# Kernel optimization log

Measured on AMD Instinct MI355X. Metric: run time of the kernel, lower is better.

Reference implementation:

```python
import jax, jax.numpy as jnp
import numpy as np

B, S, D_IN, H, G, HD = 1, 2048, 2048, 32, 8, 128
GS = H // G  # group_size = 4
D_OUT = H * HD  # 4096
EPS = 1e-6


def _rmsnorm(x, scale):
    # qwen3-compatible: compute in fp32 over last dim
    xf = x.astype(jnp.float32)
    var = jnp.mean(xf * xf, axis=-1, keepdims=True)
    return (xf * jax.lax.rsqrt(var + EPS) * scale).astype(x.dtype)


def _apply_rope(x, cos, sin):
    # x: [b, h, s, d]; cos/sin: [s, d]
    d2 = x.shape[-1] // 2
    x1, x2 = x[..., :d2], x[..., d2:]
    rotated = jnp.concatenate([-x2, x1], axis=-1)
    return (x * cos[None, None] + rotated * sin[None, None]).astype(x.dtype)


def setup_inputs() -> dict:
    key = jax.random.key(0)
    ks = jax.random.split(key, 8)
    x = jax.random.normal(ks[0], (B, S, D_IN), jnp.float32)
    mask = jnp.triu(jnp.ones((S, S), bool), k=1)  # causal: True = masked
    # RoPE tables [S, HD]
    inv_freq = 1.0 / (10000.0 ** (jnp.arange(0, HD, 2, dtype=jnp.float32) / HD))
    ang = jnp.arange(S, dtype=jnp.float32)[:, None] * inv_freq[None, :]
    ang = jnp.concatenate([ang, ang], axis=-1)
    cos, sin = jnp.cos(ang), jnp.sin(ang)
    std = 0.02
    Wq = jax.random.normal(ks[1], (D_IN, D_OUT), jnp.float32) * std
    Wk = jax.random.normal(ks[2], (D_IN, G * HD), jnp.float32) * std
    Wv = jax.random.normal(ks[3], (D_IN, G * HD), jnp.float32) * std
    Wo = jax.random.normal(ks[4], (D_OUT, D_IN), jnp.float32) * std
    q_scale = jnp.ones((HD,), jnp.float32)
    k_scale = jnp.ones((HD,), jnp.float32)
    return {"x": x, "mask": mask, "cos": cos, "sin": sin,
            "Wq": Wq, "Wk": Wk, "Wv": Wv, "Wo": Wo,
            "q_scale": q_scale, "k_scale": k_scale}


def reference(x, mask, cos, sin, Wq, Wk, Wv, Wo, q_scale, k_scale):
    b, s, _ = x.shape
    q = (x @ Wq).reshape(b, s, H, HD).transpose(0, 2, 1, 3)   # [b,H,s,hd]
    k = (x @ Wk).reshape(b, s, G, HD).transpose(0, 2, 1, 3)   # [b,G,s,hd]
    v = (x @ Wv).reshape(b, s, G, HD).transpose(0, 2, 1, 3)   # [b,G,s,hd]
    q = _rmsnorm(q, q_scale)
    k = _rmsnorm(k, k_scale)
    q = _apply_rope(q, cos[:s], sin[:s])
    k = _apply_rope(k, cos[:s], sin[:s])
    next_k, next_v = k, v  # cache (num_kv_groups heads)
    # GQA via broadcasting instead of repeat_interleave (same math)
    qg = q.reshape(b, G, GS, s, HD)
    scores = jnp.einsum('bgrsd,bgtd->bgrst', qg, k)           # [b,G,gs,s,s]
    scores = jnp.where(mask[None, None, None], -jnp.inf, scores)
    attn = jax.nn.softmax(scores / np.sqrt(HD).astype(np.float32), axis=-1)
    ctx = jnp.einsum('bgrst,bgtd->bgrsd', attn, v)            # [b,G,gs,s,hd]
    ctx = ctx.reshape(b, H, s, HD).transpose(0, 2, 1, 3).reshape(b, s, D_OUT)
    out = ctx @ Wo
    return out, next_k, next_v
```

## Files before the change

### kernel.cpp

```cpp
#include <hip/hip_runtime.h>

typedef unsigned short ushort_t;
typedef short short8 __attribute__((ext_vector_type(8)));
typedef float floatx4 __attribute__((ext_vector_type(4)));

#define S_LEN 2048
#define DIN   2048
#define NH    32
#define NG    8
#define HDIM  128
#define DOUT  4096
#define DKV   1024
#define QLD   6144

__device__ __forceinline__ float b2f(ushort_t u) {
  union { float f; unsigned u; } t; t.u = ((unsigned)u) << 16; return t.f;
}
__device__ __forceinline__ ushort_t f2b(float f) {
  union { float f; unsigned u; } t; t.f = f;
  unsigned v = t.u;
  v += 0x7FFFu + ((v >> 16) & 1u);
  return (ushort_t)(v >> 16);
}

__device__ __forceinline__ void glds16(const ushort_t* g, ushort_t* l) {
  __builtin_amdgcn_global_load_lds((const __attribute__((address_space(1))) void*)g,
                                   (__attribute__((address_space(3))) void*)l, 16, 0, 0);
}

__global__ __launch_bounds__(256) void tcast(const float* __restrict__ W,
                                             ushort_t* __restrict__ Wt,
                                             int N, int ldt) {
  __shared__ float t[32][33];
  const int bx = blockIdx.x * 32;
  const int by = blockIdx.y * 32;
  const int tx = threadIdx.x & 31;
  const int ty = threadIdx.x >> 5;
#pragma unroll
  for (int i = 0; i < 32; i += 8)
    t[ty + i][tx] = W[(size_t)(by + ty + i) * N + bx + tx];
  __syncthreads();
#pragma unroll
  for (int i = 0; i < 32; i += 8)
    Wt[(size_t)(bx + ty + i) * ldt + by + tx] = f2b(t[tx][ty + i]);
}

__global__ __launch_bounds__(256) void castx(const float* __restrict__ x,
                                             ushort_t* __restrict__ xb) {
  const size_t i = ((size_t)blockIdx.x * 256 + threadIdx.x) * 4;
  float4 v = *(const float4*)&x[i];
  union { int2 p; ushort_t s[4]; } w;
  w.s[0] = f2b(v.x); w.s[1] = f2b(v.y); w.s[2] = f2b(v.z); w.s[3] = f2b(v.w);
  *(int2*)&xb[i] = w.p;
}

template <int CF32, int BM>
__global__ __launch_bounds__(256) void gemm_glds(const ushort_t* __restrict__ A, int lda,
                                                 const ushort_t* __restrict__ Bt, int ldb,
                                                 void* __restrict__ Cp, int ldc, int K) {
  constexpr int MI = BM / 32;
  __shared__ __align__(16) ushort_t As[3][BM * 32];
  __shared__ __align__(16) ushort_t Bs[3][4096];
  const int tid  = threadIdx.x;
  const int m0   = blockIdx.y * BM;
  const int n0   = blockIdx.x * 128;
  const int wave = tid >> 6, lane = tid & 63;
  const int lrow = lane & 15, quad = lane >> 4;
  const int wm = (wave >> 1) * (BM / 2), wn = (wave & 1) * 64;

  floatx4 acc[MI][4];
#pragma unroll
  for (int mi = 0; mi < MI; mi++)
#pragma unroll
    for (int ni = 0; ni < 4; ni++)
#pragma unroll
      for (int j = 0; j < 4; j++) acc[mi][ni][j] = 0.0f;

  const int sc = ((tid & 3) ^ ((tid >> 3) & 3)) * 8;
  const ushort_t* ag0 = A + (size_t)(m0 + (tid >> 2)) * lda + sc;
  const ushort_t* ag1 = ag0 + (size_t)64 * lda;
  const ushort_t* bg0 = Bt + (size_t)(n0 + (tid >> 2)) * ldb + sc;
  const ushort_t* bg1 = bg0 + (size_t)64 * ldb;
  const int so = wave * 512;

  auto stage = [&](int k0, ushort_t* aB, ushort_t* bB) {
    glds16(ag0 + k0, aB + so);
    if constexpr (BM == 128) glds16(ag1 + k0, aB + 2048 + so);
    glds16(bg0 + k0, bB + so);
    glds16(bg1 + k0, bB + 2048 + so);
  };

  const int rq = (quad ^ ((lrow >> 1) & 3)) * 8;

  stage(0,  As[0], Bs[0]);
  stage(32, As[1], Bs[1]);
  stage(64, As[2], Bs[2]);

  ushort_t *a_cur = As[0], *a_n1 = As[1], *a_n2 = As[2];
  ushort_t *b_cur = Bs[0], *b_n1 = Bs[1], *b_n2 = Bs[2];

  const int NT = K >> 5;
  for (int t = 0; t < NT; t++) {
    if (t + 2 < NT) {
      if constexpr (BM == 128) asm volatile("s_waitcnt vmcnt(8)" ::: "memory");
      else                     asm volatile("s_waitcnt vmcnt(6)" ::: "memory");
    } else if (t + 1 < NT) {
      if constexpr (BM == 128) asm volatile("s_waitcnt vmcnt(4)" ::: "memory");
      else                     asm volatile("s_waitcnt vmcnt(3)" ::: "memory");
    } else {
      asm volatile("s_waitcnt vmcnt(0)" ::: "memory");
    }
    __builtin_amdgcn_s_barrier();

    short8 af[MI], bfr[4];
#pragma unroll
    for (int mi = 0; mi < MI; mi++)
      af[mi] = *(const short8*)&a_cur[(wm + mi * 16 + lrow) * 32 + rq];
#pragma unroll
    for (int ni = 0; ni < 4; ni++)
      bfr[ni] = *(const short8*)&b_cur[(wn + ni * 16 + lrow) * 32 + rq];
    asm volatile("s_waitcnt lgkmcnt(0)" ::: "memory");
    __builtin_amdgcn_s_barrier();

    if (t + 3 < NT) stage((t + 3) << 5, a_cur, b_cur);

    __builtin_amdgcn_s_setprio(1);
#pragma unroll
    for (int mi = 0; mi < MI; mi++)
#pragma unroll
      for (int ni = 0; ni < 4; ni++)
        acc[mi][ni] = __builtin_amdgcn_mfma_f32_16x16x32_bf16(af[mi], bfr[ni], acc[mi][ni], 0, 0, 0);
    __builtin_amdgcn_s_setprio(0);

    ushort_t* ta = a_cur; a_cur = a_n1; a_n1 = a_n2; a_n2 = ta;
    ushort_t* tb = b_cur; b_cur = b_n1; b_n1 = b_n2; b_n2 = tb;
  }
  asm volatile("s_waitcnt vmcnt(0)" ::: "memory");

#pragma unroll
  for (int mi = 0; mi < MI; mi++)
#pragma unroll
    for (int ni = 0; ni < 4; ni++)
#pragma unroll
      for (int i = 0; i < 4; i++) {
        const int row = m0 + wm + mi * 16 + quad * 4 + i;
        const int col = n0 + wn + ni * 16 + lrow;
        if (CF32) ((float*)Cp)[(size_t)row * ldc + col] = acc[mi][ni][i];
        else      ((ushort_t*)Cp)[(size_t)row * ldc + col] = f2b(acc[mi][ni][i]);
      }
}

__global__ __launch_bounds__(256) void norm_qk(ushort_t* __restrict__ qkv,
                                               const float* __restrict__ cosb,
                                               const float* __restrict__ sinb,
                                               const float* __restrict__ qs,
                                               const float* __restrict__ ks,
                                               ushort_t* __restrict__ kb) {
  const int idx  = blockIdx.x * 4 + (threadIdx.x >> 6);
  const int lane = threadIdx.x & 63;
  const int SH = S_LEN * NH;
  const float QSC = 0.08838834764831845f * 1.4426950408889634f;

  if (idx < SH) {
    const int s = idx >> 5, h = idx & 31;
    ushort_t* row = qkv + (size_t)s * QLD + h * HDIM;
    float x1 = b2f(row[lane]), x2 = b2f(row[lane + 64]);
    float ss = x1 * x1 + x2 * x2;
#pragma unroll
    for (int off = 1; off < 64; off <<= 1) ss += __shfl_xor(ss, off);
    const float inv = rsqrtf(ss * (1.0f / 128.0f) + 1e-6f);
    const float y1 = x1 * inv * qs[lane] * QSC;
    const float y2 = x2 * inv * qs[lane + 64] * QSC;
    const float c1 = cosb[s * HDIM + lane],      s1 = sinb[s * HDIM + lane];
    const float c2 = cosb[s * HDIM + lane + 64], s2 = sinb[s * HDIM + lane + 64];
    row[lane]      = f2b(y1 * c1 - y2 * s1);
    row[lane + 64] = f2b(y2 * c2 + y1 * s2);
  } else {
    const int j = idx - SH;
    const int s = j >> 3, g = j & 7;
    const ushort_t* row = qkv + (size_t)s * QLD + DOUT + g * HDIM;
    float x1 = b2f(row[lane]), x2 = b2f(row[lane + 64]);
    float ss = x1 * x1 + x2 * x2;
#pragma unroll
    for (int off = 1; off < 64; off <<= 1) ss += __shfl_xor(ss, off);
    const float inv = rsqrtf(ss * (1.0f / 128.0f) + 1e-6f);
    const float y1 = x1 * inv * ks[lane];
    const float y2 = x2 * inv * ks[lane + 64];
    const float c1 = cosb[s * HDIM + lane],      s1 = sinb[s * HDIM + lane];
    const float c2 = cosb[s * HDIM + lane + 64], s2 = sinb[s * HDIM + lane + 64];
    ushort_t* o = kb + ((size_t)g * S_LEN + s) * HDIM;
    o[lane]      = f2b(y1 * c1 - y2 * s1);
    o[lane + 64] = f2b(y2 * c2 + y1 * s2);
  }
}

__global__ __launch_bounds__(256) void vtrans(const ushort_t* __restrict__ qkv,
                                              ushort_t* __restrict__ vt) {
  __shared__ ushort_t t[64][65];
  const int g = blockIdx.x;
  const int s0 = blockIdx.y * 64, d0 = blockIdx.z * 64;
  const int tx = threadIdx.x & 63, ty = threadIdx.x >> 6;
#pragma unroll
  for (int i = 0; i < 64; i += 4)
    t[ty + i][tx] = qkv[(size_t)(s0 + ty + i) * QLD + DOUT + DKV + g * HDIM + d0 + tx];
  __syncthreads();
#pragma unroll
  for (int i = 0; i < 64; i += 4)
    vt[((size_t)(g * HDIM + d0 + ty + i)) * S_LEN + s0 + tx] = t[tx][ty + i];
}

__global__ __launch_bounds__(256, 2) void attn(ushort_t* QC,
                                               const ushort_t* __restrict__ Kb,
                                               const ushort_t* __restrict__ Vt) {
  __shared__ __align__(16) ushort_t Ks[2][8192];
  __shared__ __align__(16) ushort_t Vs[2][8192];
  __shared__ __align__(16) ushort_t Ps[64 * 72];
  const int h  = blockIdx.x;
  const int qt = 31 - blockIdx.y;
  const int g  = h >> 2;
  const int tid = threadIdx.x;
  const int wave = tid >> 6, lane = tid & 63;
  const int lrow = lane & 15, quad = lane >> 4;
  const ushort_t* Kg = Kb + (size_t)g * S_LEN * HDIM;
  const ushort_t* Vg = Vt + (size_t)g * HDIM * S_LEN;
  const int r0 = qt * 64;
  const int qrow0 = r0 + wave * 16;

  short8 qf[4];
#pragma unroll
  for (int kd = 0; kd < 4; kd++)
    qf[kd] = *(const short8*)&QC[(size_t)(qrow0 + lrow) * QLD + h * HDIM + kd * 32 + quad * 8];

  short8 vones;
#pragma unroll
  for (int j = 0; j < 8; j++) vones[j] = (lrow == 0) ? (short)0x3F80 : (short)0;

  floatx4 ctx[8], ctxl;
#pragma unroll
  for (int nd = 0; nd < 8; nd++)
#pragma unroll
    for (int j = 0; j < 4; j++) ctx[nd][j] = 0.0f;
#pragma unroll
  for (int j = 0; j < 4; j++) ctxl[j] = 0.0f;

  const int swz = ((lane & 3) ^ ((lane >> 3) & 3)) * 8;
  const ushort_t* kgl = Kg + (size_t)(wave * 16 + (lane >> 2)) * HDIM + swz;
  const ushort_t* vgl = Vg + (size_t)(wave * 32 + (lane >> 2)) * S_LEN + swz;

  auto stageKV = [&](int t0, int b) {
#pragma unroll
    for (int i = 0; i < 4; i++)
      glds16(kgl + (size_t)t0 * HDIM + i * 32, &Ks[b][i * 2048 + wave * 512]);
#pragma unroll
    for (int i = 0; i < 4; i++)
      glds16(vgl + (size_t)((i >> 1) * 16) * S_LEN + t0 + (i & 1) * 32,
             &Vs[b][(i & 1) * 4096 + (wave * 32 + (i >> 1) * 16) * 32]);
  };

  const int rq = (quad ^ ((lrow >> 1) & 3)) * 8;

  stageKV(0, 0);
  if (r0 > 0) stageKV(64, 1);

  int buf = 0;
  for (int t0 = 0; t0 <= r0; t0 += 64) {
    if (t0 < r0) asm volatile("s_waitcnt vmcnt(8)" ::: "memory");
    else         asm volatile("s_waitcnt vmcnt(0)" ::: "memory");
    __builtin_amdgcn_s_barrier();
    const ushort_t* Kc = Ks[buf];
    const ushort_t* Vc = Vs[buf];

    floatx4 sacc[4];
#pragma unroll
    for (int ni = 0; ni < 4; ni++)
#pragma unroll
      for (int j = 0; j < 4; j++) sacc[ni][j] = 0.0f;
    __builtin_amdgcn_s_setprio(1);
#pragma unroll
    for (int kd = 0; kd < 4; kd++) {
      short8 kf[4];
#pragma unroll
      for (int ni = 0; ni < 4; ni++)
        kf[ni] = *(const short8*)&Kc[kd * 2048 + (ni * 16 + lrow) * 32 + rq];
#pragma unroll
      for (int ni = 0; ni < 4; ni++)
        sacc[ni] = __builtin_amdgcn_mfma_f32_16x16x32_bf16(qf[kd], kf[ni], sacc[ni], 0, 0, 0);
    }
    __builtin_amdgcn_s_setprio(0);

    const bool diag = (t0 == r0);
#pragma unroll
    for (int ni = 0; ni < 4; ni++)
#pragma unroll
      for (int i = 0; i < 4; i++) {
        float sv = sacc[ni][i];
        if (diag && (t0 + ni * 16 + lrow > qrow0 + quad * 4 + i)) sv = -1e30f;
        sacc[ni][i] = exp2f(sv - 17.0f);
      }

#pragma unroll
    for (int ni = 0; ni < 4; ni++)
#pragma unroll
      for (int i = 0; i < 4; i++)
        Ps[(wave * 16 + quad * 4 + i) * 72 + ni * 16 + lrow] = f2b(sacc[ni][i]);
    asm volatile("s_waitcnt lgkmcnt(0)" ::: "memory");

    __builtin_amdgcn_s_setprio(1);
#pragma unroll
    for (int kt = 0; kt < 2; kt++) {
      const short8 pf = *(const short8*)&Ps[(wave * 16 + lrow) * 72 + kt * 32 + quad * 8];
      ctxl = __builtin_amdgcn_mfma_f32_16x16x32_bf16(pf, vones, ctxl, 0, 0, 0);
#pragma unroll
      for (int nd = 0; nd < 8; nd++) {
        const short8 vf = *(const short8*)&Vc[kt * 4096 + (nd * 16 + lrow) * 32 + rq];
        ctx[nd] = __builtin_amdgcn_mfma_f32_16x16x32_bf16(pf, vf, ctx[nd], 0, 0, 0);
      }
    }
    __builtin_amdgcn_s_setprio(0);

    asm volatile("s_waitcnt lgkmcnt(0)" ::: "memory");
    __builtin_amdgcn_s_barrier();
    if (t0 + 128 <= r0) stageKV(t0 + 128, buf);
    buf ^= 1;
  }

  float invl[4];
#pragma unroll
  for (int i = 0; i < 4; i++) invl[i] = 1.0f / __shfl(ctxl[i], lane & 48);

  asm volatile("s_waitcnt vmcnt(0)" ::: "memory");
  __syncthreads();
  ushort_t* Es = (wave < 2) ? Ks[0] : Vs[0];
  const int eb = (wave & 1) * 16;
#pragma unroll
  for (int i = 0; i < 4; i++)
#pragma unroll
    for (int nd = 0; nd < 8; nd++)
      Es[(eb + quad * 4 + i) * 136 + nd * 16 + lrow] = f2b(ctx[nd][i] * invl[i]);
  asm volatile("s_waitcnt lgkmcnt(0)" ::: "memory");
  const int erow = lane >> 4;
  const int ecol = (lane & 15) * 8;
#pragma unroll
  for (int rr = 0; rr < 4; rr++) {
    int4 v = *(const int4*)&Es[(eb + rr * 4 + erow) * 136 + ecol];
    *(int4*)&QC[(size_t)(r0 + wave * 16 + rr * 4 + erow) * QLD + h * HDIM + ecol] = v;
  }
}

__global__ __launch_bounds__(256) void fink(const ushort_t* __restrict__ kb,
                                            float* __restrict__ nk) {
  const size_t e = ((size_t)blockIdx.x * 256 + threadIdx.x) * 8;
  union { int4 v; ushort_t s[8]; } u;
  u.v = *(const int4*)&kb[e];
#pragma unroll
  for (int j = 0; j < 8; j++) nk[e + j] = b2f(u.s[j]);
}

__global__ __launch_bounds__(256) void finv(const ushort_t* __restrict__ qkv,
                                            float* __restrict__ nv) {
  const int s = blockIdx.x;
  const int g = threadIdx.x >> 5, d4 = (threadIdx.x & 31) * 4;
  union { short4 v; ushort_t s[4]; } u;
  u.v = *(const short4*)&qkv[(size_t)s * QLD + DOUT + DKV + g * HDIM + d4];
  float4 o;
  o.x = b2f(u.s[0]); o.y = b2f(u.s[1]); o.z = b2f(u.s[2]); o.w = b2f(u.s[3]);
  *(float4*)&nv[((size_t)g * S_LEN + s) * HDIM + d4] = o;
}

extern "C" void kernel_launch(void* const* d_in, const int* in_sizes, int n_in,
                              void* d_out, int out_size, void* d_ws, size_t ws_size,
                              hipStream_t stream) {
  const float* x    = (const float*)d_in[0];
  const float* cosb = (const float*)d_in[2];
  const float* sinb = (const float*)d_in[3];
  const float* Wq   = (const float*)d_in[4];
  const float* Wk   = (const float*)d_in[5];
  const float* Wv   = (const float*)d_in[6];
  const float* Wo   = (const float*)d_in[7];
  const float* qs   = (const float*)d_in[8];
  const float* ks   = (const float*)d_in[9];

  float* outf = (float*)d_out;
  float* nkf  = outf + (size_t)S_LEN * DIN;
  float* nvf  = nkf + (size_t)NG * S_LEN * HDIM;

  const size_t MiB = 1024 * 1024;
  ushort_t* WallT = (ushort_t*)d_out;
  ushort_t* xb    = (ushort_t*)((char*)d_out + 24 * MiB);
  ushort_t* WoT   = (ushort_t*)((char*)d_out + 16 * MiB);
  ushort_t* vt    = (ushort_t*)d_out;
  ushort_t* qkv   = (ushort_t*)d_ws;
  ushort_t* kb    = (ushort_t*)((char*)d_ws + 24 * MiB);

  tcast<<<dim3(128, 64), 256, 0, stream>>>(Wq, WallT, DOUT, DIN);
  tcast<<<dim3(32, 64), 256, 0, stream>>>(Wk, WallT + (size_t)4096 * DIN, DKV, DIN);
  tcast<<<dim3(32, 64), 256, 0, stream>>>(Wv, WallT + (size_t)5120 * DIN, DKV, DIN);
  castx<<<4096, 256, 0, stream>>>(x, xb);

  gemm_glds<0, 128><<<dim3(48, 16), 256, 0, stream>>>(xb, DIN, WallT, DIN, qkv, QLD, DIN);

  tcast<<<dim3(64, 128), 256, 0, stream>>>(Wo, WoT, DIN, DOUT);

  norm_qk<<<(S_LEN * NH + S_LEN * NG) / 4, 256, 0, stream>>>(qkv, cosb, sinb, qs, ks, kb);

  vtrans<<<dim3(NG, S_LEN / 64, HDIM / 64), 256, 0, stream>>>(qkv, vt);

  attn<<<dim3(NH, 32), 256, 0, stream>>>(qkv, kb, vt);

  gemm_glds<1, 64><<<dim3(16, 32), 256, 0, stream>>>(qkv, QLD, WoT, DOUT, outf, DIN, DOUT);

  fink<<<1024, 256, 0, stream>>>(kb, nkf);
  finv<<<S_LEN, 256, 0, stream>>>(qkv, nvf);
}
```

Measured before the change: 376.9 us.

## Enlarge attention tiles to 128 query rows with split K/V triple-buffered pipeline

Each attention block now handles 128 query rows with 8 waves instead of 64 rows with 4, so every staged K/V tile is shared by twice as many waves. K and V loads are issued separately through a rotating pool of three LDS slots. The next V tile is prefetched during QK^T and the next K tile during PV. Waves whose rows lie entirely before a key tile skip it, and the query-tile ordering is changed to balance causal work across blocks. The cost is more barriers per iteration and heavier per-block resource use at the higher launch bound.

```diff
diff --git a/kernel.cpp b/kernel.cpp
--- a/kernel.cpp
+++ b/kernel.cpp
@@ -209,22 +209,23 @@
     vt[((size_t)(g * HDIM + d0 + ty + i)) * S_LEN + s0 + tx] = t[tx][ty + i];
 }
 
-__global__ __launch_bounds__(256, 2) void attn(ushort_t* QC,
+__global__ __launch_bounds__(512, 4) void attn(ushort_t* QC,
                                                const ushort_t* __restrict__ Kb,
                                                const ushort_t* __restrict__ Vt) {
-  __shared__ __align__(16) ushort_t Ks[2][8192];
-  __shared__ __align__(16) ushort_t Vs[2][8192];
-  __shared__ __align__(16) ushort_t Ps[64 * 72];
+  __shared__ __align__(16) ushort_t pool[3 * 8192];
+  __shared__ __align__(16) ushort_t Ps[128 * 72];
   const int h  = blockIdx.x;
-  const int qt = 31 - blockIdx.y;
+  const int y  = blockIdx.y;
+  const int qt = (y < 8) ? (15 - y) : (y - 8);
   const int g  = h >> 2;
   const int tid = threadIdx.x;
   const int wave = tid >> 6, lane = tid & 63;
   const int lrow = lane & 15, quad = lane >> 4;
   const ushort_t* Kg = Kb + (size_t)g * S_LEN * HDIM;
   const ushort_t* Vg = Vt + (size_t)g * HDIM * S_LEN;
-  const int r0 = qt * 64;
+  const int r0 = qt * 128;
   const int qrow0 = r0 + wave * 16;
+  const int L = 2 * qt + 1;
 
   short8 qf[4];
 #pragma unroll
@@ -244,84 +245,98 @@
   for (int j = 0; j < 4; j++) ctxl[j] = 0.0f;
 
   const int swz = ((lane & 3) ^ ((lane >> 3) & 3)) * 8;
-  const ushort_t* kgl = Kg + (size_t)(wave * 16 + (lane >> 2)) * HDIM + swz;
-  const ushort_t* vgl = Vg + (size_t)(wave * 32 + (lane >> 2)) * S_LEN + swz;
-
-  auto stageKV = [&](int t0, int b) {
-#pragma unroll
-    for (int i = 0; i < 4; i++)
-      glds16(kgl + (size_t)t0 * HDIM + i * 32, &Ks[b][i * 2048 + wave * 512]);
-#pragma unroll
-    for (int i = 0; i < 4; i++)
-      glds16(vgl + (size_t)((i >> 1) * 16) * S_LEN + t0 + (i & 1) * 32,
-             &Vs[b][(i & 1) * 4096 + (wave * 32 + (i >> 1) * 16) * 32]);
+  auto stageK = [&](int t0, ushort_t* slot) {
+#pragma unroll
+    for (int j = 0; j < 2; j++) {
+      const int rgrp = 2 * (wave & 1) + j;
+      glds16(Kg + (size_t)(t0 + rgrp * 16 + (lane >> 2)) * HDIM + (wave >> 1) * 32 + swz,
+             slot + (wave >> 1) * 2048 + rgrp * 512);
+    }
   };
+  auto stageV = [&](int t0, ushort_t* slot) {
+#pragma unroll
+    for (int j = 0; j < 2; j++)
+      glds16(Vg + (size_t)(wave * 16 + (lane >> 2)) * S_LEN + t0 + j * 32 + swz,
+             slot + j * 4096 + wave * 512);
+  };
 
   const int rq = (quad ^ ((lrow >> 1) & 3)) * 8;
 
-  stageKV(0, 0);
-  if (r0 > 0) stageKV(64, 1);
-
-  int buf = 0;
-  for (int t0 = 0; t0 <= r0; t0 += 64) {
-    if (t0 < r0) asm volatile("s_waitcnt vmcnt(8)" ::: "memory");
-    else         asm volatile("s_waitcnt vmcnt(0)" ::: "memory");
-    __builtin_amdgcn_s_barrier();
-    const ushort_t* Kc = Ks[buf];
-    const ushort_t* Vc = Vs[buf];
+  ushort_t *pK = pool, *pV = pool + 8192, *pN = pool + 16384;
+  stageK(0, pK); stageV(0, pV); stageK(64, pN);
+  asm volatile("s_waitcnt vmcnt(4)" ::: "memory");
+  __builtin_amdgcn_s_barrier();
+
+  for (int t = 0; t <= L; t++) {
+    const int t0 = t * 64;
+    const bool skip   = (t0 > qrow0 + 15);
+    const bool domask = (t0 + 63 > qrow0);
 
     floatx4 sacc[4];
-#pragma unroll
-    for (int ni = 0; ni < 4; ni++)
-#pragma unroll
-      for (int j = 0; j < 4; j++) sacc[ni][j] = 0.0f;
-    __builtin_amdgcn_s_setprio(1);
-#pragma unroll
-    for (int kd = 0; kd < 4; kd++) {
-      short8 kf[4];
+    if (!skip) {
 #pragma unroll
       for (int ni = 0; ni < 4; ni++)
-        kf[ni] = *(const short8*)&Kc[kd * 2048 + (ni * 16 + lrow) * 32 + rq];
-#pragma unroll
-      for (int ni = 0; ni < 4; ni++)
-        sacc[ni] = __builtin_amdgcn_mfma_f32_16x16x32_bf16(qf[kd], kf[ni], sacc[ni], 0, 0, 0);
-    }
-    __builtin_amdgcn_s_setprio(0);
-
-    const bool diag = (t0 == r0);
-#pragma unroll
-    for (int ni = 0; ni < 4; ni++)
-#pragma unroll
-      for (int i = 0; i < 4; i++) {
-        float sv = sacc[ni][i];
-        if (diag && (t0 + ni * 16 + lrow > qrow0 + quad * 4 + i)) sv = -1e30f;
-        sacc[ni][i] = exp2f(sv - 17.0f);
+#pragma unroll
+        for (int j = 0; j < 4; j++) sacc[ni][j] = 0.0f;
+      __builtin_amdgcn_s_setprio(1);
+#pragma unroll
+      for (int kd = 0; kd < 4; kd++) {
+        short8 kf[4];
+#pragma unroll
+        for (int ni = 0; ni < 4; ni++)
+          kf[ni] = *(const short8*)&pK[kd * 2048 + (ni * 16 + lrow) * 32 + rq];
+#pragma unroll
+        for (int ni = 0; ni < 4; ni++)
+          sacc[ni] = __builtin_amdgcn_mfma_f32_16x16x32_bf16(qf[kd], kf[ni], sacc[ni], 0, 0, 0);
       }
-
-#pragma unroll
-    for (int ni = 0; ni < 4; ni++)
-#pragma unroll
-      for (int i = 0; i < 4; i++)
-        Ps[(wave * 16 + quad * 4 + i) * 72 + ni * 16 + lrow] = f2b(sacc[ni][i]);
-    asm volatile("s_waitcnt lgkmcnt(0)" ::: "memory");
-
-    __builtin_amdgcn_s_setprio(1);
-#pragma unroll
-    for (int kt = 0; kt < 2; kt++) {
-      const short8 pf = *(const short8*)&Ps[(wave * 16 + lrow) * 72 + kt * 32 + quad * 8];
-      ctxl = __builtin_amdgcn_mfma_f32_16x16x32_bf16(pf, vones, ctxl, 0, 0, 0);
-#pragma unroll
-      for (int nd = 0; nd < 8; nd++) {
-        const short8 vf = *(const short8*)&Vc[kt * 4096 + (nd * 16 + lrow) * 32 + rq];
-        ctx[nd] = __builtin_amdgcn_mfma_f32_16x16x32_bf16(pf, vf, ctx[nd], 0, 0, 0);
-      }
-    }
-    __builtin_amdgcn_s_setprio(0);
-
+      __builtin_amdgcn_s_setprio(0);
+    }
     asm volatile("s_waitcnt lgkmcnt(0)" ::: "memory");
     __builtin_amdgcn_s_barrier();
-    if (t0 + 128 <= r0) stageKV(t0 + 128, buf);
-    buf ^= 1;
+    if (t < L) stageV(t0 + 64, pK);
+
+    if (!skip) {
+#pragma unroll
+      for (int ni = 0; ni < 4; ni++)
+#pragma unroll
+        for (int i = 0; i < 4; i++) {
+          float sv = sacc[ni][i];
+          if (domask && (t0 + ni * 16 + lrow > qrow0 + quad * 4 + i)) sv = -1e30f;
+          sacc[ni][i] = exp2f(sv - 17.0f);
+        }
+#pragma unroll
+      for (int ni = 0; ni < 4; ni++)
+#pragma unroll
+        for (int i = 0; i < 4; i++)
+          Ps[(wave * 16 + quad * 4 + i) * 72 + ni * 16 + lrow] = f2b(sacc[ni][i]);
+      asm volatile("s_waitcnt lgkmcnt(0)" ::: "memory");
+    }
+
+    if (t < L) asm volatile("s_waitcnt vmcnt(4)" ::: "memory");
+    else       asm volatile("s_waitcnt vmcnt(0)" ::: "memory");
+    __builtin_amdgcn_s_barrier();
+
+    if (!skip) {
+      __builtin_amdgcn_s_setprio(1);
+#pragma unroll
+      for (int kt = 0; kt < 2; kt++) {
+        const short8 pf = *(const short8*)&Ps[(wave * 16 + lrow) * 72 + kt * 32 + quad * 8];
+        ctxl = __builtin_amdgcn_mfma_f32_16x16x32_bf16(pf, vones, ctxl, 0, 0, 0);
+#pragma unroll
+        for (int nd = 0; nd < 8; nd++) {
+          const short8 vf = *(const short8*)&pV[kt * 4096 + (nd * 16 + lrow) * 32 + rq];
+          ctx[nd] = __builtin_amdgcn_mfma_f32_16x16x32_bf16(pf, vf, ctx[nd], 0, 0, 0);
+        }
+      }
+      __builtin_amdgcn_s_setprio(0);
+    }
+
+    if (t < L) {
+      asm volatile("s_waitcnt lgkmcnt(0) vmcnt(2)" ::: "memory");
+      __builtin_amdgcn_s_barrier();
+      if (t + 2 <= L) stageK(t0 + 128, pV);
+      ushort_t* t1 = pK; pK = pN; pN = pV; pV = t1;
+    }
   }
 
   float invl[4];
@@ -330,20 +345,19 @@
 
   asm volatile("s_waitcnt vmcnt(0)" ::: "memory");
   __syncthreads();
-  ushort_t* Es = (wave < 2) ? Ks[0] : Vs[0];
-  const int eb = (wave & 1) * 16;
+  ushort_t* Es = pool + wave * 2176;
 #pragma unroll
   for (int i = 0; i < 4; i++)
 #pragma unroll
     for (int nd = 0; nd < 8; nd++)
-      Es[(eb + quad * 4 + i) * 136 + nd * 16 + lrow] = f2b(ctx[nd][i] * invl[i]);
+      Es[(quad * 4 + i) * 136 + nd * 16 + lrow] = f2b(ctx[nd][i] * invl[i]);
   asm volatile("s_waitcnt lgkmcnt(0)" ::: "memory");
   const int erow = lane >> 4;
   const int ecol = (lane & 15) * 8;
 #pragma unroll
   for (int rr = 0; rr < 4; rr++) {
-    int4 v = *(const int4*)&Es[(eb + rr * 4 + erow) * 136 + ecol];
-    *(int4*)&QC[(size_t)(r0 + wave * 16 + rr * 4 + erow) * QLD + h * HDIM + ecol] = v;
+    int4 v = *(const int4*)&Es[(rr * 4 + erow) * 136 + ecol];
+    *(int4*)&QC[(size_t)(qrow0 + rr * 4 + erow) * QLD + h * HDIM + ecol] = v;
   }
 }
 
@@ -405,7 +419,7 @@
 
   vtrans<<<dim3(NG, S_LEN / 64, HDIM / 64), 256, 0, stream>>>(qkv, vt);
 
-  attn<<<dim3(NH, 32), 256, 0, stream>>>(qkv, kb, vt);
+  attn<<<dim3(NH, 16), 512, 0, stream>>>(qkv, kb, vt);
 
   gemm_glds<1, 64><<<dim3(16, 32), 256, 0, stream>>>(qkv, QLD, WoT, DOUT, outf, DIN, DOUT);
 
```

Result: no change. 380.7 us (+1.0%).
